# Kernel tuning notes

Measured on AMD Instinct MI355X. Metric: run time of the kernel, lower is better.

The kernel has to match this reference:

```python
import jax, jax.numpy as jnp
import numpy as np

BN_EPS = 1e-5


def maxpool2(x):
    # 2x2 max pool, stride 2: (B,C,H,W) -> (B,C,H//2,W//2)
    B, C, H, W = x.shape
    return x.reshape(B, C, H // 2, 2, W // 2, 2).max(axis=(3, 5))


def setup_inputs() -> dict:
    key = jax.random.key(0)
    ks = jax.random.split(key, 6)
    B, C, H, W = 4, 64, 96, 96   # in_dim = 64
    K, OD = 64, 64               # key_dim, out_dim
    sc = lambda fan: 1.0 / np.sqrt(fan)
    return {
        "c2": jax.random.normal(ks[0], (B, C, H, W), jnp.float32),
        "x": jax.random.normal(ks[1], (B, C, H, W), jnp.float32),
        # edge_att: Conv2d(2C->OD, 1x1, no bias) -> BN -> ReLU -> Conv2d(OD->1, 1x1) -> Sigmoid
        "w_ea1": jax.random.normal(ks[2], (OD, 2 * C), jnp.float32) * sc(2 * C),
        "bn_w": jnp.ones((OD,), jnp.float32),
        "bn_b": jnp.zeros((OD,), jnp.float32),
        "bn_m": jnp.zeros((OD,), jnp.float32),
        "bn_v": jnp.ones((OD,), jnp.float32),
        "w_ea2": jax.random.normal(ks[3], (1, OD), jnp.float32) * sc(OD),
        "b_ea2": jnp.zeros((1,), jnp.float32),
        # query_conv (shared for query AND key in the original forward)
        "w_q": jax.random.normal(ks[4], (K, C), jnp.float32) * sc(C),
        "b_q": jnp.zeros((K,), jnp.float32),
        "gamma": jnp.full((1,), 0.5, jnp.float32),
    }


def reference(c2, x, w_ea1, bn_w, bn_b, bn_m, bn_v, w_ea2, b_ea2, w_q, b_q, gamma):
    xp = maxpool2(x)        # (B,C,Hp,Wp)
    c2p = maxpool2(c2)
    B, C, H, W = x.shape
    Hp, Wp = xp.shape[2], xp.shape[3]

    # edge attention gate on pooled features -> (B,1,Hp,Wp)
    cat = jnp.concatenate([c2p, xp], axis=1)                       # (B,2C,Hp,Wp)
    h = jnp.einsum('oc,bchw->bohw', w_ea1, cat)
    bn_scale = (bn_w / jnp.sqrt(bn_v + BN_EPS))[None, :, None, None]
    h = jax.nn.relu((h - bn_m[None, :, None, None]) * bn_scale + bn_b[None, :, None, None])
    ea = jax.nn.sigmoid(jnp.einsum('oc,bchw->bohw', w_ea2, h) + b_ea2[None, :, None, None])

    # query at full res, key at pooled res (SAME conv weights, as in the source)
    q = jnp.einsum('kc,bchw->bkhw', w_q, x) + b_q[None, :, None, None]    # (B,K,H,W)
    k = jnp.einsum('kc,bchw->bkhw', w_q, xp) + b_q[None, :, None, None]   # (B,K,Hp,Wp)

    pq = q.reshape(B, -1, H * W)        # (B,K,N)
    pk = k.reshape(B, -1, Hp * Wp)      # (B,K,M)
    energy = jnp.einsum('bkn,bkm->bnm', pq, pk)                    # (B,N,M)
    attn = jax.nn.softmax(energy * ea.reshape(B, 1, Hp * Wp), axis=-1)

    v = xp.reshape(B, C, Hp * Wp)                                   # (B,C,M)
    out = jnp.einsum('bcm,bnm->bcn', v, attn).reshape(B, C, H, W)
    return gamma[0] * out + x
```

## Files before the change

kernel.cpp:

```cpp
#include <hip/hip_runtime.h>
#include <stdint.h>

#define B_ 4
#define C_ 64
#define H_ 96
#define W_ 96
#define HP_ 48
#define WP_ 48
#define N_ (H_*W_)
#define M_ (HP_*WP_)
#define KD_ 64
#define OD_ 64
#define BN_EPS 1e-5f
#define LOG2E 1.4426950408889634f
#define SHIFT2 28.853900817779268f
#define QT_ 48
#define QI_ (QT_/16)
#define QB_ (N_/QT_)
#define NT_ (M_/64)

typedef __bf16 bf16_t;
typedef bf16_t bf16x8 __attribute__((ext_vector_type(8)));
typedef bf16_t bf16x4 __attribute__((ext_vector_type(4)));
typedef float f32x4 __attribute__((ext_vector_type(4)));
typedef short short4v __attribute__((ext_vector_type(4)));

static __device__ __forceinline__ unsigned short f2bf(float f) {
    unsigned int u = __builtin_bit_cast(unsigned int, f);
    u += 0x7fffu + ((u >> 16) & 1u);
    return (unsigned short)(u >> 16);
}

static __device__ __forceinline__ f32x4 mfma16_bf16(short4v a, short4v b, f32x4 c) {
#if __has_builtin(__builtin_amdgcn_mfma_f32_16x16x16bf16_1k)
    return __builtin_amdgcn_mfma_f32_16x16x16bf16_1k(a, b, c, 0, 0, 0);
#else
    return c;
#endif
}

static __device__ __forceinline__ void gl_lds16(const unsigned short* g, unsigned short* l) {
#if __has_builtin(__builtin_amdgcn_global_load_lds)
    __builtin_amdgcn_global_load_lds(
        (const __attribute__((address_space(1))) unsigned int*)(const void*)g,
        (__attribute__((address_space(3))) unsigned int*)(void*)l, 16, 0, 0);
#endif
}

static __device__ __forceinline__ void setprio1() {
#if __has_builtin(__builtin_amdgcn_s_setprio)
    __builtin_amdgcn_s_setprio(1);
#endif
}
static __device__ __forceinline__ void setprio0() {
#if __has_builtin(__builtin_amdgcn_s_setprio)
    __builtin_amdgcn_s_setprio(0);
#endif
}
static __device__ __forceinline__ void schedbar0() {
#if __has_builtin(__builtin_amdgcn_sched_barrier)
    __builtin_amdgcn_sched_barrier(0);
#endif
}
static __device__ __forceinline__ void rawbar() {
#if __has_builtin(__builtin_amdgcn_s_barrier)
    __builtin_amdgcn_s_barrier();
#else
    __syncthreads();
#endif
}

__global__ __launch_bounds__(256) void prep_kernel(
    const float* __restrict__ x, const float* __restrict__ c2,
    const float* __restrict__ wq, const float* __restrict__ bq,
    const float* __restrict__ w1, const float* __restrict__ bnw, const float* __restrict__ bnb,
    const float* __restrict__ bnm, const float* __restrict__ bnv,
    const float* __restrict__ w2, const float* __restrict__ b2,
    unsigned short* __restrict__ kb, unsigned short* __restrict__ vb, float* __restrict__ ea) {

    __shared__ float lw1[OD_*2*C_];
    __shared__ float lwq[KD_*C_];
    __shared__ float xs[C_*33];
    __shared__ float c2s[C_*33];
    __shared__ float red[8][32];

    int tid = threadIdx.x;
    int b = blockIdx.x / 72;
    int m0 = (blockIdx.x % 72) * 32;

    for (int i = tid; i < OD_*2*C_; i += 256) lw1[i] = w1[i];
    for (int i = tid; i < KD_*C_; i += 256) lwq[i] = wq[i];
    for (int j = tid; j < 2048; j += 256) {
        int c = j >> 5, p = j & 31;
        int m = m0 + p;
        int hp = m / WP_, wp = m % WP_;
        size_t base = ((size_t)(b*C_ + c)*H_ + 2*hp)*W_ + 2*wp;
        const float* px = x + base;
        float mx = fmaxf(fmaxf(px[0], px[1]), fmaxf(px[W_], px[W_+1]));
        xs[c*33 + p] = mx;
        vb[(size_t)(b*C_ + c)*M_ + m] = f2bf(mx);
        const float* pc = c2 + base;
        c2s[c*33 + p] = fmaxf(fmaxf(pc[0], pc[1]), fmaxf(pc[W_], pc[W_+1]));
    }
    __syncthreads();

    int ml = tid & 31, oz = tid >> 5;
    int m = m0 + ml;

    float h[8] = {0,0,0,0,0,0,0,0};
    for (int c = 0; c < C_; c += 4) {
        float x0 = xs[c*33+ml], x1 = xs[(c+1)*33+ml], x2 = xs[(c+2)*33+ml], x3 = xs[(c+3)*33+ml];
        #pragma unroll
        for (int oi = 0; oi < 8; oi++) {
            const float4 wv = *(const float4*)&lwq[(oz*8 + oi)*C_ + c];
            h[oi] = fmaf(wv.x, x0, fmaf(wv.y, x1, fmaf(wv.z, x2, fmaf(wv.w, x3, h[oi]))));
        }
    }
    unsigned short tmp[8];
    #pragma unroll
    for (int oi = 0; oi < 8; oi++) tmp[oi] = f2bf(h[oi] + bq[oz*8 + oi]);
    *(uint4*)&kb[((size_t)b*M_ + m)*KD_ + oz*8] = *(const uint4*)tmp;

    float g[8] = {0,0,0,0,0,0,0,0};
    for (int c = 0; c < 2*C_; c += 4) {
        const float* srcb = (c < C_) ? &c2s[c*33] : &xs[(c - C_)*33];
        float x0 = srcb[ml], x1 = srcb[33+ml], x2 = srcb[66+ml], x3 = srcb[99+ml];
        #pragma unroll
        for (int oi = 0; oi < 8; oi++) {
            const float4 wv = *(const float4*)&lw1[(oz*8 + oi)*(2*C_) + c];
            g[oi] = fmaf(wv.x, x0, fmaf(wv.y, x1, fmaf(wv.z, x2, fmaf(wv.w, x3, g[oi]))));
        }
    }
    float z = 0.f;
    #pragma unroll
    for (int oi = 0; oi < 8; oi++) {
        int o = oz*8 + oi;
        float sc = bnw[o] * rsqrtf(bnv[o] + BN_EPS);
        float t = (g[oi] - bnm[o]) * sc + bnb[o];
        z += w2[o] * fmaxf(t, 0.f);
    }
    red[oz][ml] = z;
    __syncthreads();
    if (oz == 0) {
        float s = b2[0];
        #pragma unroll
        for (int i = 0; i < 8; i++) s += red[i][ml];
        ea[(size_t)b*M_ + m] = LOG2E / (1.f + __builtin_amdgcn_exp2f(-s * LOG2E));
    }
}

__global__ __launch_bounds__(256) void qk_kernel(const float* __restrict__ in, const float* __restrict__ wq,
    const float* __restrict__ bq, unsigned short* __restrict__ outb) {
    __shared__ float lw[KD_*C_];
    for (int i = threadIdx.x; i < KD_*C_; i += 256) lw[i] = wq[i];
    __syncthreads();
    int ml = threadIdx.x & 31, oz = threadIdx.x >> 5;
    int pg = blockIdx.x * 32 + ml;
    float h[8] = {0,0,0,0,0,0,0,0};
    const float* src = in + ((size_t)(pg / N_))*C_*N_ + (pg % N_);
    for (int c = 0; c < C_; c += 4) {
        float x0 = src[(size_t)c*N_], x1 = src[(size_t)(c+1)*N_];
        float x2 = src[(size_t)(c+2)*N_], x3 = src[(size_t)(c+3)*N_];
        #pragma unroll
        for (int oi = 0; oi < 8; oi++) {
            const float4 wv = *(const float4*)&lw[(oz*8 + oi)*C_ + c];
            h[oi] = fmaf(wv.x, x0, fmaf(wv.y, x1, fmaf(wv.z, x2, fmaf(wv.w, x3, h[oi]))));
        }
    }
    unsigned short tmp[8];
    #pragma unroll
    for (int oi = 0; oi < 8; oi++) tmp[oi] = f2bf(h[oi] + bq[oz*8 + oi]);
    *(uint4*)&outb[(size_t)pg*KD_ + oz*8] = *(const uint4*)tmp;
}

__global__ __launch_bounds__(256, 3) void attn_kernel(
    const unsigned short* __restrict__ qb, const unsigned short* __restrict__ kb,
    const unsigned short* __restrict__ vb, const float* __restrict__ ea,
    const float* __restrict__ x, const float* __restrict__ gamma_p, float* __restrict__ out) {

    __shared__ __align__(16) char smem[41984];

    int tid = threadIdx.x;
    int wave = tid >> 6, lane = tid & 63, quad = lane >> 4, l16 = lane & 15;
    int blk = blockIdx.x;
    int b = (blk & 7) >> 1;
    int n_base = ((blk & 1) * (QB_/2) + (blk >> 3)) * QT_;

    bf16x8 qf[QI_][2];
    #pragma unroll
    for (int qi = 0; qi < QI_; qi++) {
        const unsigned short* qp = qb + ((size_t)b*N_ + n_base + qi*16 + l16)*KD_;
        qf[qi][0] = __builtin_bit_cast(bf16x8, *(const uint4*)(qp + quad*8));
        qf[qi][1] = __builtin_bit_cast(bf16x8, *(const uint4*)(qp + 32 + quad*8));
    }

    f32x4 o2[QI_][4];
    f32x4 lacc[QI_];
    #pragma unroll
    for (int qi = 0; qi < QI_; qi++) {
        lacc[qi] = (f32x4){0.f,0.f,0.f,0.f};
        #pragma unroll
        for (int ct = 0; ct < 4; ct++) o2[qi][ct] = (f32x4){0.f,0.f,0.f,0.f};
    }
    const short one_bf = (short)0x3F80;
    short4v ones = (short4v){one_bf, one_bf, one_bf, one_bf};

    const unsigned short* kbB = kb + (size_t)b*M_*KD_;
    const unsigned short* vbB = vb + (size_t)b*C_*M_;
    const float* eaB = ea + (size_t)b*M_;

    int srow = tid >> 3;
    int ksw  = ((tid & 7) ^ (srow & 7)) << 3;

    auto STAGE = [&](int mb, char* kd, char* vd) {
        unsigned short* kds = (unsigned short*)kd;
        unsigned short* vds = (unsigned short*)vd;
        gl_lds16(kbB + (size_t)(mb + srow)*KD_      + ksw, kds + tid*8);
        gl_lds16(kbB + (size_t)(mb + srow + 32)*KD_ + ksw, kds + 2048 + tid*8);
        gl_lds16(vbB + (size_t)srow*M_      + mb + ksw, vds + tid*8);
        gl_lds16(vbB + (size_t)(srow+32)*M_ + mb + ksw, vds + 2048 + tid*8);
    };

    {
        const f32x4* eaV = (const f32x4*)eaB;
        f32x4* eaL = (f32x4*)(smem + 32768);
        for (int i = tid; i < M_/4; i += 256) eaL[i] = eaV[i];
    }
    STAGE(0,  smem,          smem + 8192);
    STAGE(64, smem + 16384,  smem + 16384 + 8192);
    asm volatile("s_waitcnt vmcnt(4)" ::: "memory");
    asm volatile("s_waitcnt lgkmcnt(0)" ::: "memory");
    rawbar();
    asm volatile("" ::: "memory");

    const float* lds_ea = (const float*)(smem + 32768);
    int xsw = l16 & 7;
    int krow = wave*16 + l16;

    struct FragSet { bf16x8 kf0, kf1; short4v va0, va1, va2, va3; f32x4 e4; };
    FragSet fA, fB;

    {
        unsigned short* kc = (unsigned short*)smem;
        unsigned short* vc = (unsigned short*)(smem + 8192);
        fA.e4  = *(const f32x4*)&lds_ea[0*64 + wave*16 + quad*4];
        fA.kf0 = __builtin_bit_cast(bf16x8, *(const uint4*)(kc + krow*KD_ + (((quad  ) ^ xsw) << 3)));
        fA.kf1 = __builtin_bit_cast(bf16x8, *(const uint4*)(kc + krow*KD_ + (((quad+4) ^ xsw) << 3)));
        fA.va0 = *(const short4v*)(vc + (0*16 + l16)*64 + (((wave*2 + (quad>>1)) ^ xsw) << 3) + (quad&1)*4);
        fA.va1 = *(const short4v*)(vc + (1*16 + l16)*64 + (((wave*2 + (quad>>1)) ^ xsw) << 3) + (quad&1)*4);
        fA.va2 = *(const short4v*)(vc + (2*16 + l16)*64 + (((wave*2 + (quad>>1)) ^ xsw) << 3) + (quad&1)*4);
        fA.va3 = *(const short4v*)(vc + (3*16 + l16)*64 + (((wave*2 + (quad>>1)) ^ xsw) << 3) + (quad&1)*4);
    }

#define ATTN_STEP(T_, CUR, NXT)                                                        \
    {                                                                                  \
        const int t_ = (T_);                                                           \
        if (t_ < NT_ - 1) {                                                            \
            asm volatile("s_waitcnt vmcnt(0)" ::: "memory");   \
            schedbar0();                                                               \
            rawbar();                                \
            asm volatile("" ::: "memory");                                             \
            schedbar0();                                                               \
            if (t_ + 2 < NT_) {                                                        \
                char* nb = smem + (t_ & 1) * 16384;                                    \
                STAGE((t_ + 2) * 64, nb, nb + 8192);                                   \
            }                                                                          \
            unsigned short* kc_ = (unsigned short*)(smem + ((t_ + 1) & 1) * 16384);    \
            unsigned short* vc_ = (unsigned short*)(smem + ((t_ + 1) & 1) * 16384 + 8192); \
            NXT.e4  = *(const f32x4*)&lds_ea[(t_ + 1)*64 + wave*16 + quad*4];          \
            NXT.kf0 = __builtin_bit_cast(bf16x8, *(const uint4*)(kc_ + krow*KD_ + (((quad  ) ^ xsw) << 3))); \
            NXT.kf1 = __builtin_bit_cast(bf16x8, *(const uint4*)(kc_ + krow*KD_ + (((quad+4) ^ xsw) << 3))); \
            NXT.va0 = *(const short4v*)(vc_ + (0*16 + l16)*64 + (((wave*2 + (quad>>1)) ^ xsw) << 3) + (quad&1)*4); \
            NXT.va1 = *(const short4v*)(vc_ + (1*16 + l16)*64 + (((wave*2 + (quad>>1)) ^ xsw) << 3) + (quad&1)*4); \
            NXT.va2 = *(const short4v*)(vc_ + (2*16 + l16)*64 + (((wave*2 + (quad>>1)) ^ xsw) << 3) + (quad&1)*4); \
            NXT.va3 = *(const short4v*)(vc_ + (3*16 + l16)*64 + (((wave*2 + (quad>>1)) ^ xsw) << 3) + (quad&1)*4); \
            schedbar0();                                                               \
            asm volatile("s_waitcnt lgkmcnt(7)" ::: "memory");   \
            schedbar0();                                                               \
        } else {                                                                       \
            schedbar0();                                                               \
            asm volatile("s_waitcnt lgkmcnt(0)" ::: "memory");      \
            schedbar0();                                                               \
        }                                                                              \
                               \
        f32x4 st[QI_];                                                                 \
        setprio1();                                                                    \
        _Pragma("unroll")                                                              \
        for (int qi = 0; qi < QI_; qi++) {                                             \
            f32x4 z = (f32x4){0.f,0.f,0.f,0.f};                                        \
            z = __builtin_amdgcn_mfma_f32_16x16x32_bf16(CUR.kf0, qf[qi][0], z, 0, 0, 0); \
            z = __builtin_amdgcn_mfma_f32_16x16x32_bf16(CUR.kf1, qf[qi][1], z, 0, 0, 0); \
            st[qi] = z;                                                                \
        }                                                                              \
        setprio0();                                                                    \
        short4v pk[QI_];                                                               \
        _Pragma("unroll")                                                              \
        for (int qi = 0; qi < QI_; qi++) {                                             \
            f32x4 p;                                                                   \
            p[0] = __builtin_amdgcn_exp2f(fmaf(st[qi][0], CUR.e4[0], -SHIFT2));        \
            p[1] = __builtin_amdgcn_exp2f(fmaf(st[qi][1], CUR.e4[1], -SHIFT2));        \
            p[2] = __builtin_amdgcn_exp2f(fmaf(st[qi][2], CUR.e4[2], -SHIFT2));        \
            p[3] = __builtin_amdgcn_exp2f(fmaf(st[qi][3], CUR.e4[3], -SHIFT2));        \
            pk[qi] = __builtin_bit_cast(short4v, __builtin_convertvector(p, bf16x4));  \
        }                                                                              \
        setprio1();                                                                    \
        _Pragma("unroll")                                                              \
        for (int qi = 0; qi < QI_; qi++) {                                             \
            o2[qi][0] = mfma16_bf16(CUR.va0, pk[qi], o2[qi][0]);                       \
            o2[qi][1] = mfma16_bf16(CUR.va1, pk[qi], o2[qi][1]);                       \
            o2[qi][2] = mfma16_bf16(CUR.va2, pk[qi], o2[qi][2]);                       \
            o2[qi][3] = mfma16_bf16(CUR.va3, pk[qi], o2[qi][3]);                       \
            lacc[qi]  = mfma16_bf16(ones,    pk[qi], lacc[qi]);                        \
        }                                                                              \
        setprio0();                                                                    \
    }

    for (int t = 0; t < NT_; t += 2) {
        ATTN_STEP(t,     fA, fB);
        ATTN_STEP(t + 1, fB, fA);
    }
#undef ATTN_STEP

    __syncthreads();

    float* o_red0 = (float*)smem;
    float* o_red1 = o_red0 + QT_*68;
    float* l_red  = o_red1 + QT_*68;

    if (lane < 16) {
        #pragma unroll
        for (int qi = 0; qi < QI_; qi++) l_red[wave*QT_ + qi*16 + l16] = lacc[qi][0];
    }
    if (wave < 2) {
        float* od = (wave == 0) ? o_red0 : o_red1;
        #pragma unroll
        for (int qi = 0; qi < QI_; qi++)
            #pragma unroll
            for (int ct = 0; ct < 4; ct++)
                *(f32x4*)&od[(qi*16 + l16)*68 + ct*16 + quad*4] = o2[qi][ct];
    }
    __syncthreads();
    if (wave >= 2) {
        float* od = (wave == 2) ? o_red0 : o_red1;
        #pragma unroll
        for (int qi = 0; qi < QI_; qi++)
            #pragma unroll
            for (int ct = 0; ct < 4; ct++) {
                f32x4* p = (f32x4*)&od[(qi*16 + l16)*68 + ct*16 + quad*4];
                *p += o2[qi][ct];
            }
    }
    __syncthreads();
    if (tid < QT_) {
        float s = (l_red[tid] + l_red[QT_ + tid]) + (l_red[2*QT_ + tid] + l_red[3*QT_ + tid]);
        l_red[tid] = 1.f / s;
    }
    __syncthreads();

    float gmm = gamma_p[0];
    int c = tid >> 2, q4 = tid & 3;
    const float* xrow = x + ((size_t)b*C_ + c)*N_ + n_base;
    float* orow = out + ((size_t)b*C_ + c)*N_ + n_base;
    #pragma unroll
    for (int i = 0; i < QI_; i++) {
        int q0 = q4*4 + i*16;
        float4 xv = *(const float4*)(xrow + q0);
        float4 ov;
        float v0 = (o_red0[(q0+0)*68 + c] + o_red1[(q0+0)*68 + c]) * l_red[q0+0];
        float v1 = (o_red0[(q0+1)*68 + c] + o_red1[(q0+1)*68 + c]) * l_red[q0+1];
        float v2 = (o_red0[(q0+2)*68 + c] + o_red1[(q0+2)*68 + c]) * l_red[q0+2];
        float v3 = (o_red0[(q0+3)*68 + c] + o_red1[(q0+3)*68 + c]) * l_red[q0+3];
        ov.x = fmaf(gmm, v0, xv.x);
        ov.y = fmaf(gmm, v1, xv.y);
        ov.z = fmaf(gmm, v2, xv.z);
        ov.w = fmaf(gmm, v3, xv.w);
        *(float4*)(orow + q0) = ov;
    }
}

extern "C" void kernel_launch(void* const* d_in, const int* in_sizes, int n_in,
                              void* d_out, int out_size, void* d_ws, size_t ws_size,
                              hipStream_t stream) {
    const float* c2    = (const float*)d_in[0];
    const float* x     = (const float*)d_in[1];
    const float* w_ea1 = (const float*)d_in[2];
    const float* bn_w  = (const float*)d_in[3];
    const float* bn_b  = (const float*)d_in[4];
    const float* bn_m  = (const float*)d_in[5];
    const float* bn_v  = (const float*)d_in[6];
    const float* w_ea2 = (const float*)d_in[7];
    const float* b_ea2 = (const float*)d_in[8];
    const float* w_q   = (const float*)d_in[9];
    const float* b_q   = (const float*)d_in[10];
    const float* gamma = (const float*)d_in[11];
    float* out = (float*)d_out;

    char* ws = (char*)d_ws;
    float* ea            = (float*)(ws + 0);
    unsigned short* qb   = (unsigned short*)(ws + 36864);
    unsigned short* kb   = (unsigned short*)(ws + 4755456);
    unsigned short* vb   = (unsigned short*)(ws + 5935104);

    prep_kernel<<<dim3((B_*M_)/32), dim3(256), 0, stream>>>(x, c2, w_q, b_q,
        w_ea1, bn_w, bn_b, bn_m, bn_v, w_ea2, b_ea2, kb, vb, ea);
    qk_kernel<<<dim3((B_*N_)/32), dim3(256), 0, stream>>>(x, w_q, b_q, qb);
    attn_kernel<<<dim3(B_*QB_), dim3(256), 0, stream>>>(qb, kb, vb, ea, x, gamma, out);
}
```

Before: 160.6 us.

## Use per-wave private triple-buffered K/V staging to remove block barriers

Each wave now stages only the K rows, V columns and edge-attention values it consumes into its own LDS region. The buffering goes from double to triple, and the vmcnt waits are per wave with no block-wide s_barrier in the main loop. The goal is to drop the per-tile workgroup synchronisation and the upfront copy of the whole ea vector, and to deepen the prefetch. In exchange there are more, smaller global-to-LDS loads per wave, and the LDS footprint changes (about 50KB versus 42KB), which may affect occupancy at 3 blocks per CU.

```diff
diff --git a/kernel.cpp b/kernel.cpp
--- a/kernel.cpp
+++ b/kernel.cpp
@@ -19,6 +19,10 @@
 #define QB_ (N_/QT_)
 #define NT_ (M_/64)
 
+#define WSTR_ 4160
+#define BUFSTR_ 16640
+#define SMEM_ (3*BUFSTR_)
+
 typedef __bf16 bf16_t;
 typedef bf16_t bf16x8 __attribute__((ext_vector_type(8)));
 typedef bf16_t bf16x4 __attribute__((ext_vector_type(4)));
@@ -60,13 +64,6 @@
 static __device__ __forceinline__ void schedbar0() {
 #if __has_builtin(__builtin_amdgcn_sched_barrier)
     __builtin_amdgcn_sched_barrier(0);
-#endif
-}
-static __device__ __forceinline__ void rawbar() {
-#if __has_builtin(__builtin_amdgcn_s_barrier)
-    __builtin_amdgcn_s_barrier();
-#else
-    __syncthreads();
 #endif
 }
 
@@ -178,7 +175,7 @@
     const unsigned short* __restrict__ vb, const float* __restrict__ ea,
     const float* __restrict__ x, const float* __restrict__ gamma_p, float* __restrict__ out) {
 
-    __shared__ __align__(16) char smem[41984];
+    __shared__ __align__(16) char smem[SMEM_];
 
     int tid = threadIdx.x;
     int wave = tid >> 6, lane = tid & 63, quad = lane >> 4, l16 = lane & 15;
@@ -209,80 +206,87 @@
     const unsigned short* vbB = vb + (size_t)b*C_*M_;
     const float* eaB = ea + (size_t)b*M_;
 
-    int srow = tid >> 3;
-    int ksw  = ((tid & 7) ^ (srow & 7)) << 3;
-
-    auto STAGE = [&](int mb, char* kd, char* vd) {
-        unsigned short* kds = (unsigned short*)kd;
-        unsigned short* vds = (unsigned short*)vd;
-        gl_lds16(kbB + (size_t)(mb + srow)*KD_      + ksw, kds + tid*8);
-        gl_lds16(kbB + (size_t)(mb + srow + 32)*KD_ + ksw, kds + 2048 + tid*8);
-        gl_lds16(vbB + (size_t)srow*M_      + mb + ksw, vds + tid*8);
-        gl_lds16(vbB + (size_t)(srow+32)*M_ + mb + ksw, vds + 2048 + tid*8);
+    const unsigned short* kSrc = kbB + (size_t)(wave*16 + (lane>>3))*KD_
+                                     + (((lane&7) ^ (lane>>3)) << 3);
+    const unsigned short* vSrc = vbB + (size_t)(lane>>1)*M_ + wave*16
+                                     + (((lane&1) ^ ((lane>>3)&1)) << 3);
+    char* wbW = smem + wave*WSTR_;
+
+    auto STAGE = [&](int mb, char* wbuf) {
+        unsigned short* kd = (unsigned short*)wbuf;
+        unsigned short* vd = (unsigned short*)(wbuf + 2048);
+        unsigned short* ed = (unsigned short*)(wbuf + 4096);
+        gl_lds16(kSrc + (size_t)mb*KD_,          kd + lane*8);
+        gl_lds16(kSrc + (size_t)(mb + 8)*KD_,    kd + 512 + lane*8);
+        gl_lds16(vSrc + mb,                      vd + lane*8);
+        gl_lds16(vSrc + mb + (size_t)32*M_,      vd + 512 + lane*8);
+        if (lane < 4)
+            gl_lds16((const unsigned short*)(eaB + mb + wave*16) + lane*8, ed + lane*8);
     };
 
-    {
-        const f32x4* eaV = (const f32x4*)eaB;
-        f32x4* eaL = (f32x4*)(smem + 32768);
-        for (int i = tid; i < M_/4; i += 256) eaL[i] = eaV[i];
-    }
-    STAGE(0,  smem,          smem + 8192);
-    STAGE(64, smem + 16384,  smem + 16384 + 8192);
-    asm volatile("s_waitcnt vmcnt(4)" ::: "memory");
-    asm volatile("s_waitcnt lgkmcnt(0)" ::: "memory");
-    rawbar();
-    asm volatile("" ::: "memory");
-
-    const float* lds_ea = (const float*)(smem + 32768);
-    int xsw = l16 & 7;
-    int krow = wave*16 + l16;
+    STAGE(0,   wbW);
+    STAGE(64,  wbW + BUFSTR_);
+    STAGE(128, wbW + 2*BUFSTR_);
+    asm volatile("s_waitcnt vmcnt(10)" ::: "memory");
+    schedbar0();
+
+    int xsw  = l16 & 7;
+    int kOff0 = l16*64 + ((quad ^ xsw) << 3);
+    int kOff1 = l16*64 + (((quad + 4) ^ xsw) << 3);
+    int vsw  = (l16 >> 2) & 1;
+    int vOff0 = (0*16 + l16)*16 + ((((quad>>1) ^ vsw)) << 3) + (quad&1)*4;
+    int vOff1 = (1*16 + l16)*16 + ((((quad>>1) ^ vsw)) << 3) + (quad&1)*4;
+    int vOff2 = (2*16 + l16)*16 + ((((quad>>1) ^ vsw)) << 3) + (quad&1)*4;
+    int vOff3 = (3*16 + l16)*16 + ((((quad>>1) ^ vsw)) << 3) + (quad&1)*4;
 
     struct FragSet { bf16x8 kf0, kf1; short4v va0, va1, va2, va3; f32x4 e4; };
     FragSet fA, fB;
 
     {
-        unsigned short* kc = (unsigned short*)smem;
-        unsigned short* vc = (unsigned short*)(smem + 8192);
-        fA.e4  = *(const f32x4*)&lds_ea[0*64 + wave*16 + quad*4];
-        fA.kf0 = __builtin_bit_cast(bf16x8, *(const uint4*)(kc + krow*KD_ + (((quad  ) ^ xsw) << 3)));
-        fA.kf1 = __builtin_bit_cast(bf16x8, *(const uint4*)(kc + krow*KD_ + (((quad+4) ^ xsw) << 3)));
-        fA.va0 = *(const short4v*)(vc + (0*16 + l16)*64 + (((wave*2 + (quad>>1)) ^ xsw) << 3) + (quad&1)*4);
-        fA.va1 = *(const short4v*)(vc + (1*16 + l16)*64 + (((wave*2 + (quad>>1)) ^ xsw) << 3) + (quad&1)*4);
-        fA.va2 = *(const short4v*)(vc + (2*16 + l16)*64 + (((wave*2 + (quad>>1)) ^ xsw) << 3) + (quad&1)*4);
-        fA.va3 = *(const short4v*)(vc + (3*16 + l16)*64 + (((wave*2 + (quad>>1)) ^ xsw) << 3) + (quad&1)*4);
-    }
-
-#define ATTN_STEP(T_, CUR, NXT)                                                        \
+        unsigned short* kc_ = (unsigned short*)wbW;
+        unsigned short* vc_ = (unsigned short*)(wbW + 2048);
+        const float*    ec_ = (const float*)(wbW + 4096);
+        fA.e4  = *(const f32x4*)(ec_ + quad*4);
+        fA.kf0 = __builtin_bit_cast(bf16x8, *(const uint4*)(kc_ + kOff0));
+        fA.kf1 = __builtin_bit_cast(bf16x8, *(const uint4*)(kc_ + kOff1));
+        fA.va0 = *(const short4v*)(vc_ + vOff0);
+        fA.va1 = *(const short4v*)(vc_ + vOff1);
+        fA.va2 = *(const short4v*)(vc_ + vOff2);
+        fA.va3 = *(const short4v*)(vc_ + vOff3);
+    }
+    asm volatile("s_waitcnt lgkmcnt(0)" ::: "memory");
+    schedbar0();
+
+#define ATTN_STEP(T_, CUR, NXT, RB_, SB_)                                              \
     {                                                                                  \
         const int t_ = (T_);                                                           \
         if (t_ < NT_ - 1) {                                                            \
-            asm volatile("s_waitcnt vmcnt(0)" ::: "memory");   \
-            schedbar0();                                                               \
-            rawbar();                                \
-            asm volatile("" ::: "memory");                                             \
-            schedbar0();                                                               \
-            if (t_ + 2 < NT_) {                                                        \
-                char* nb = smem + (t_ & 1) * 16384;                                    \
-                STAGE((t_ + 2) * 64, nb, nb + 8192);                                   \
+            if (t_ + 2 < NT_) { asm volatile("s_waitcnt vmcnt(5)" ::: "memory"); }     \
+            else              { asm volatile("s_waitcnt vmcnt(0)" ::: "memory"); }     \
+            schedbar0();                                                               \
+            {                                                                          \
+                char* wbR = wbW + (RB_)*BUFSTR_;                                       \
+                unsigned short* kc_ = (unsigned short*)wbR;                            \
+                unsigned short* vc_ = (unsigned short*)(wbR + 2048);                   \
+                const float*    ec_ = (const float*)(wbR + 4096);                      \
+                NXT.e4  = *(const f32x4*)(ec_ + quad*4);                               \
+                NXT.kf0 = __builtin_bit_cast(bf16x8, *(const uint4*)(kc_ + kOff0));    \
+                NXT.kf1 = __builtin_bit_cast(bf16x8, *(const uint4*)(kc_ + kOff1));    \
+                NXT.va0 = *(const short4v*)(vc_ + vOff0);                              \
+                NXT.va1 = *(const short4v*)(vc_ + vOff1);                              \
+                NXT.va2 = *(const short4v*)(vc_ + vOff2);                              \
+                NXT.va3 = *(const short4v*)(vc_ + vOff3);                              \
             }                                                                          \
-            unsigned short* kc_ = (unsigned short*)(smem + ((t_ + 1) & 1) * 16384);    \
-            unsigned short* vc_ = (unsigned short*)(smem + ((t_ + 1) & 1) * 16384 + 8192); \
-            NXT.e4  = *(const f32x4*)&lds_ea[(t_ + 1)*64 + wave*16 + quad*4];          \
-            NXT.kf0 = __builtin_bit_cast(bf16x8, *(const uint4*)(kc_ + krow*KD_ + (((quad  ) ^ xsw) << 3))); \
-            NXT.kf1 = __builtin_bit_cast(bf16x8, *(const uint4*)(kc_ + krow*KD_ + (((quad+4) ^ xsw) << 3))); \
-            NXT.va0 = *(const short4v*)(vc_ + (0*16 + l16)*64 + (((wave*2 + (quad>>1)) ^ xsw) << 3) + (quad&1)*4); \
-            NXT.va1 = *(const short4v*)(vc_ + (1*16 + l16)*64 + (((wave*2 + (quad>>1)) ^ xsw) << 3) + (quad&1)*4); \
-            NXT.va2 = *(const short4v*)(vc_ + (2*16 + l16)*64 + (((wave*2 + (quad>>1)) ^ xsw) << 3) + (quad&1)*4); \
-            NXT.va3 = *(const short4v*)(vc_ + (3*16 + l16)*64 + (((wave*2 + (quad>>1)) ^ xsw) << 3) + (quad&1)*4); \
+            schedbar0();                                                               \
+            if (t_ + 3 < NT_) { STAGE((t_ + 3)*64, wbW + (SB_)*BUFSTR_); }             \
             schedbar0();                                                               \
             asm volatile("s_waitcnt lgkmcnt(7)" ::: "memory");   \
             schedbar0();                                                               \
         } else {                                                                       \
             schedbar0();                                                               \
-            asm volatile("s_waitcnt lgkmcnt(0)" ::: "memory");      \
+            asm volatile("s_waitcnt lgkmcnt(0)" ::: "memory");                         \
             schedbar0();                                                               \
         }                                                                              \
-                               \
         f32x4 st[QI_];                                                                 \
         setprio1();                                                                    \
         _Pragma("unroll")                                                              \
@@ -315,9 +319,13 @@
         setprio0();                                                                    \
     }
 
-    for (int t = 0; t < NT_; t += 2) {
-        ATTN_STEP(t,     fA, fB);
-        ATTN_STEP(t + 1, fB, fA);
+    for (int base = 0; base < NT_; base += 6) {
+        ATTN_STEP(base + 0, fA, fB, 1, 0);
+        ATTN_STEP(base + 1, fB, fA, 2, 1);
+        ATTN_STEP(base + 2, fA, fB, 0, 2);
+        ATTN_STEP(base + 3, fB, fA, 1, 0);
+        ATTN_STEP(base + 4, fA, fB, 2, 1);
+        ATTN_STEP(base + 5, fB, fA, 0, 2);
     }
 #undef ATTN_STEP
 
```

Result: slower. 172.3 us (+7.3%).

## Fuse query projection into attention kernel via LDS staging

Applied to the files above, without the earlier changes.

Removes the separate qk_kernel launch and its global bf16 Q buffer. Each attention block now loads w_q into LDS, computes its own 48 query rows from x, and writes them swizzled into LDS before loading the MFMA fragments. This saves a kernel launch and a global write/read round trip. In exchange each block adds a prologue with weight loading, an extra barrier, and reuse of shared memory that delays K/V staging.

```diff
diff --git a/kernel.cpp b/kernel.cpp
--- a/kernel.cpp
+++ b/kernel.cpp
@@ -149,34 +149,11 @@
     }
 }
 
-__global__ __launch_bounds__(256) void qk_kernel(const float* __restrict__ in, const float* __restrict__ wq,
-    const float* __restrict__ bq, unsigned short* __restrict__ outb) {
-    __shared__ float lw[KD_*C_];
-    for (int i = threadIdx.x; i < KD_*C_; i += 256) lw[i] = wq[i];
-    __syncthreads();
-    int ml = threadIdx.x & 31, oz = threadIdx.x >> 5;
-    int pg = blockIdx.x * 32 + ml;
-    float h[8] = {0,0,0,0,0,0,0,0};
-    const float* src = in + ((size_t)(pg / N_))*C_*N_ + (pg % N_);
-    for (int c = 0; c < C_; c += 4) {
-        float x0 = src[(size_t)c*N_], x1 = src[(size_t)(c+1)*N_];
-        float x2 = src[(size_t)(c+2)*N_], x3 = src[(size_t)(c+3)*N_];
-        #pragma unroll
-        for (int oi = 0; oi < 8; oi++) {
-            const float4 wv = *(const float4*)&lw[(oz*8 + oi)*C_ + c];
-            h[oi] = fmaf(wv.x, x0, fmaf(wv.y, x1, fmaf(wv.z, x2, fmaf(wv.w, x3, h[oi]))));
-        }
-    }
-    unsigned short tmp[8];
-    #pragma unroll
-    for (int oi = 0; oi < 8; oi++) tmp[oi] = f2bf(h[oi] + bq[oz*8 + oi]);
-    *(uint4*)&outb[(size_t)pg*KD_ + oz*8] = *(const uint4*)tmp;
-}
-
 __global__ __launch_bounds__(256, 3) void attn_kernel(
-    const unsigned short* __restrict__ qb, const unsigned short* __restrict__ kb,
-    const unsigned short* __restrict__ vb, const float* __restrict__ ea,
-    const float* __restrict__ x, const float* __restrict__ gamma_p, float* __restrict__ out) {
+    const float* __restrict__ wq, const float* __restrict__ bq,
+    const unsigned short* __restrict__ kb, const unsigned short* __restrict__ vb,
+    const float* __restrict__ ea, const float* __restrict__ x,
+    const float* __restrict__ gamma_p, float* __restrict__ out) {
 
     __shared__ __align__(16) char smem[41984];
 
@@ -185,13 +162,61 @@
     int blk = blockIdx.x;
     int b = (blk & 7) >> 1;
     int n_base = ((blk & 1) * (QB_/2) + (blk >> 3)) * QT_;
+    int xsw = l16 & 7;
+
+    float* lwq = (float*)smem;
+    unsigned short* qlds = (unsigned short*)(smem + 16384);
+    for (int i = tid; i < KD_*C_; i += 256) lwq[i] = wq[i];
+    __syncthreads();
+    {
+        const float* xb = x + (size_t)b*C_*N_ + n_base;
+        {
+            int ml = tid & 31, oz = tid >> 5;
+            float h[8] = {0,0,0,0,0,0,0,0};
+            const float* src = xb + ml;
+            for (int c = 0; c < C_; c += 4) {
+                float x0 = src[(size_t)c*N_], x1 = src[(size_t)(c+1)*N_];
+                float x2 = src[(size_t)(c+2)*N_], x3 = src[(size_t)(c+3)*N_];
+                #pragma unroll
+                for (int oi = 0; oi < 8; oi++) {
+                    const float4 wv = *(const float4*)&lwq[(oz*8 + oi)*C_ + c];
+                    h[oi] = fmaf(wv.x, x0, fmaf(wv.y, x1, fmaf(wv.z, x2, fmaf(wv.w, x3, h[oi]))));
+                }
+            }
+            unsigned short tmp[8];
+            #pragma unroll
+            for (int oi = 0; oi < 8; oi++) tmp[oi] = f2bf(h[oi] + bq[oz*8 + oi]);
+            *(uint4*)&qlds[ml*64 + ((oz ^ (ml & 7)) << 3)] = *(const uint4*)tmp;
+        }
+        {
+            int ml = tid & 15, kq = tid >> 4;
+            int n_l = 32 + ml;
+            float h[4] = {0,0,0,0};
+            const float* src = xb + n_l;
+            for (int c = 0; c < C_; c += 4) {
+                float x0 = src[(size_t)c*N_], x1 = src[(size_t)(c+1)*N_];
+                float x2 = src[(size_t)(c+2)*N_], x3 = src[(size_t)(c+3)*N_];
+                #pragma unroll
+                for (int oi = 0; oi < 4; oi++) {
+                    const float4 wv = *(const float4*)&lwq[(kq*4 + oi)*C_ + c];
+                    h[oi] = fmaf(wv.x, x0, fmaf(wv.y, x1, fmaf(wv.z, x2, fmaf(wv.w, x3, h[oi]))));
+                }
+            }
+            unsigned short tmp[4];
+            #pragma unroll
+            for (int oi = 0; oi < 4; oi++) tmp[oi] = f2bf(h[oi] + bq[kq*4 + oi]);
+            *(uint2*)&qlds[n_l*64 + (((kq >> 1) ^ (n_l & 7)) << 3) + (kq & 1)*4] =
+                *(const uint2*)tmp;
+        }
+    }
+    __syncthreads();
 
     bf16x8 qf[QI_][2];
     #pragma unroll
     for (int qi = 0; qi < QI_; qi++) {
-        const unsigned short* qp = qb + ((size_t)b*N_ + n_base + qi*16 + l16)*KD_;
-        qf[qi][0] = __builtin_bit_cast(bf16x8, *(const uint4*)(qp + quad*8));
-        qf[qi][1] = __builtin_bit_cast(bf16x8, *(const uint4*)(qp + 32 + quad*8));
+        const unsigned short* qp = qlds + (qi*16 + l16)*64;
+        qf[qi][0] = __builtin_bit_cast(bf16x8, *(const uint4*)(qp + ((quad     ^ xsw) << 3)));
+        qf[qi][1] = __builtin_bit_cast(bf16x8, *(const uint4*)(qp + (((quad+4) ^ xsw) << 3)));
     }
 
     f32x4 o2[QI_][4];
@@ -226,15 +251,15 @@
         f32x4* eaL = (f32x4*)(smem + 32768);
         for (int i = tid; i < M_/4; i += 256) eaL[i] = eaV[i];
     }
+    asm volatile("s_waitcnt lgkmcnt(0)" ::: "memory");
+    __syncthreads();
     STAGE(0,  smem,          smem + 8192);
     STAGE(64, smem + 16384,  smem + 16384 + 8192);
     asm volatile("s_waitcnt vmcnt(4)" ::: "memory");
-    asm volatile("s_waitcnt lgkmcnt(0)" ::: "memory");
     rawbar();
     asm volatile("" ::: "memory");
 
     const float* lds_ea = (const float*)(smem + 32768);
-    int xsw = l16 & 7;
     int krow = wave*16 + l16;
 
     struct FragSet { bf16x8 kf0, kf1; short4v va0, va1, va2, va3; f32x4 e4; };
@@ -397,12 +422,10 @@
 
     char* ws = (char*)d_ws;
     float* ea            = (float*)(ws + 0);
-    unsigned short* qb   = (unsigned short*)(ws + 36864);
-    unsigned short* kb   = (unsigned short*)(ws + 4755456);
-    unsigned short* vb   = (unsigned short*)(ws + 5935104);
+    unsigned short* kb   = (unsigned short*)(ws + 36864);
+    unsigned short* vb   = (unsigned short*)(ws + 1216512);
 
     prep_kernel<<<dim3((B_*M_)/32), dim3(256), 0, stream>>>(x, c2, w_q, b_q,
         w_ea1, bn_w, bn_b, bn_m, bn_v, w_ea2, b_ea2, kb, vb, ea);
-    qk_kernel<<<dim3((B_*N_)/32), dim3(256), 0, stream>>>(x, w_q, b_q, qb);
-    attn_kernel<<<dim3(B_*QB_), dim3(256), 0, stream>>>(qb, kb, vb, ea, x, gamma, out);
-}
+    attn_kernel<<<dim3(B_*QB_), dim3(256), 0, stream>>>(w_q, b_q, kb, vb, ea, x, gamma, out);
+}
```

Measured after the change: 152.3 us. -5.2%, faster.
